# Kernel tuning notes

Measured on AMD Instinct MI355X. Metric: run time of the kernel, lower is better.

## Reference

```python
import jax, jax.numpy as jnp
import numpy as np

THRESHOLD = 1.0
CURRENT_DECAY = 0.5
VOLTAGE_DECAY = 0.5
WEIGHT_SCALE = 2.0  # slayer block weight_scale=2, weight_norm=False


def spike_fn(v):
    # Heaviside spike with hard threshold (forward only)
    return (v >= THRESHOLD).astype(v.dtype)


def conv_transpose_2d(x, w):
    # x: [NT, Cin, H, W]; w: [Cin, Cout, k, k] (pytorch ConvTranspose2d layout)
    # Equivalent dilated conv: swap in/out, flip spatial taps.
    rhs = jnp.transpose(w, (1, 0, 2, 3))[:, :, ::-1, ::-1]
    return jax.lax.conv_general_dilated(
        x, rhs, window_strides=(1, 1), padding=[(1, 1), (1, 1)],
        lhs_dilation=(2, 2), dimension_numbers=('NCHW', 'OIHW', 'NCHW'))


def cuba_block(x, w):
    # x: [N, Cin, H, W, T] -> spikes [N, Cout, 2H-1, 2W-1, T]
    N, Cin, H, W, T = x.shape
    xt = jnp.transpose(x, (4, 0, 1, 2, 3)).reshape(T * N, Cin, H, W)
    z = conv_transpose_2d(xt, WEIGHT_SCALE * w)  # synapse over all timesteps at once
    Cout, Ho, Wo = z.shape[1], z.shape[2], z.shape[3]
    z = z.reshape(T, N, Cout, Ho, Wo)

    def step(carry, zt):
        cur, vol = carry
        cur = (1.0 - CURRENT_DECAY) * cur + zt          # CUBA current dynamics
        vol = (1.0 - VOLTAGE_DECAY) * vol + cur          # CUBA voltage dynamics
        s = spike_fn(vol)
        vol = vol * (1.0 - s)                            # reset voltage on spike
        return (cur, vol), s

    init = (jnp.zeros_like(z[0]), jnp.zeros_like(z[0]))
    _, spikes = jax.lax.scan(step, init, z)              # [T, N, Cout, Ho, Wo]
    return jnp.transpose(spikes, (1, 2, 3, 4, 0))


def setup_inputs() -> dict:
    key = jax.random.key(0)
    k1, k2, k3, k4 = jax.random.split(key, 4)
    c_hid, C = 32, 2
    spike = (jax.random.uniform(k1, (4, c_hid * 4, 16, 16, 32)) < 0.3).astype(jnp.float32)

    def winit(k, cin, cout):
        return jax.random.normal(k, (cin, cout, 3, 3), jnp.float32) / np.sqrt(cin * 9.0)

    return {
        'spike': spike,
        'w1': winit(k2, c_hid * 4, c_hid * 2),
        'w2': winit(k3, c_hid * 2, c_hid),
        'w3': winit(k4, c_hid, C),
    }


def reference(spike, w1, w2, w3):
    counts = []
    for w in (w1, w2, w3):
        spike = cuba_block(spike, w)
        counts.append(jnp.mean(spike))
    return spike, jnp.stack(counts).reshape(1, -1)
```

## Files before the change

kernel.cpp:

```cpp
#include <hip/hip_runtime.h>

#define TT 32

__device__ __forceinline__ float bf16_bits_to_f32(unsigned short u) {
    unsigned v = ((unsigned)u) << 16; float f; __builtin_memcpy(&f, &v, 4); return f;
}
__device__ __forceinline__ unsigned short f32_to_bf16_rne(float f) {
    unsigned u; __builtin_memcpy(&u, &f, 4);
    u += 0x7FFFu + ((u >> 16) & 1u);
    return (unsigned short)(u >> 16);
}
__device__ __forceinline__ float round_bf16_f32(float f) {
    return bf16_bits_to_f32(f32_to_bf16_rne(f));
}
__device__ __forceinline__ float f64_to_bf16_f32(double d) {
    float fz = __double2float_rz(d);
    if ((double)fz != d) {
        unsigned u; __builtin_memcpy(&u, &fz, 4); u |= 1u; __builtin_memcpy(&fz, &u, 4);
    }
    return round_bf16_f32(fz);
}
__device__ __forceinline__ unsigned spread4(unsigned b) {
    unsigned x = (b | (b << 12)) & 0x000F000Fu;
    x = (x | (x << 6)) & 0x03030303u;
    x = (x | (x << 3)) & 0x11111111u;
    return x;
}

__global__ void detect_and_init(const unsigned* __restrict__ spk,
                                int* __restrict__ flag, float* __restrict__ sums)
{
    unsigned w = spk[threadIdx.x];
    bool ok = (w == 0u) || (w == 0x3F800000u);
    unsigned long long vote = __ballot(ok);
    if (threadIdx.x == 0) {
        flag[0] = (vote == 0xFFFFFFFFFFFFFFFFull) ? 0 : 1;
        sums[0] = 0.f; sums[1] = 0.f; sums[2] = 0.f;
    }
}

__global__ __launch_bounds__(256)
void pack_interleave(const void* __restrict__ ginv, unsigned* __restrict__ idx0,
                     const int* __restrict__ flag)
{
    const int gid = blockIdx.x * 256 + threadIdx.x;
    if (gid >= 32768) return;
    const int site = gid & 255;
    const int g    = (gid >> 8) & 31;
    const int n    = gid >> 13;

    unsigned m[4];
    #pragma unroll
    for (int k = 0; k < 4; ++k) {
        const size_t ebase = ((size_t)(n * 128 + 4 * g + k) * 256 + site) * TT;
        unsigned mask = 0u;
        if (flag[0]) {
            const uint4* p = (const uint4*)((const unsigned short*)ginv + ebase);
            #pragma unroll
            for (int q = 0; q < 4; ++q) {
                uint4 a = p[q];
                unsigned wd[4] = {a.x, a.y, a.z, a.w};
                #pragma unroll
                for (int mm = 0; mm < 4; ++mm) {
                    const int t = q * 8 + mm * 2;
                    mask |= (wd[mm] & 0xFFFFu) ? (1u << t)       : 0u;
                    mask |= (wd[mm] >> 16)     ? (1u << (t + 1)) : 0u;
                }
            }
        } else {
            const float4* p = (const float4*)((const float*)ginv + ebase);
            #pragma unroll
            for (int j = 0; j < 8; ++j) {
                float4 v = p[j];
                mask |= (v.x != 0.f) ? (1u << (j * 4 + 0)) : 0u;
                mask |= (v.y != 0.f) ? (1u << (j * 4 + 1)) : 0u;
                mask |= (v.z != 0.f) ? (1u << (j * 4 + 2)) : 0u;
                mask |= (v.w != 0.f) ? (1u << (j * 4 + 3)) : 0u;
            }
        }
        m[k] = mask;
    }
    #pragma unroll
    for (int q = 0; q < 4; ++q) {
        const unsigned w =  spread4((m[0] >> (8 * q)) & 0xFFu)
                         | (spread4((m[1] >> (8 * q)) & 0xFFu) << 1)
                         | (spread4((m[2] >> (8 * q)) & 0xFFu) << 2)
                         | (spread4((m[3] >> (8 * q)) & 0xFFu) << 3);
        idx0[q * 32768 + gid] = w;
    }
}

template<int C, int PLANE>
__global__ __launch_bounds__(256)
void pack_mid(const unsigned* __restrict__ masks, unsigned* __restrict__ idx)
{
    constexpr int G = C / 4;
    constexpr int TOT = 4 * G * PLANE;
    const int gid = blockIdx.x * 256 + threadIdx.x;
    if (gid >= TOT) return;
    const int site = gid % PLANE;
    const int g    = (gid / PLANE) % G;
    const int n    = gid / (PLANE * G);
    unsigned m[4];
    #pragma unroll
    for (int k = 0; k < 4; ++k)
        m[k] = masks[(n * C + 4 * g + k) * PLANE + site];
    #pragma unroll
    for (int q = 0; q < 4; ++q) {
        const unsigned w =  spread4((m[0] >> (8 * q)) & 0xFFu)
                         | (spread4((m[1] >> (8 * q)) & 0xFFu) << 1)
                         | (spread4((m[2] >> (8 * q)) & 0xFFu) << 2)
                         | (spread4((m[3] >> (8 * q)) & 0xFFu) << 3);
        idx[q * TOT + gid] = w;
    }
}

template<int CIN, int COUT, int MODE, bool LAST>
__global__ __launch_bounds__(256, 4)
void cuba_layer(const unsigned* __restrict__ idxIn, const void* __restrict__ wptr,
                void* __restrict__ goutv, unsigned* __restrict__ maskOut,
                int N, int Hi, int Wi, float* __restrict__ sumOut,
                const int* __restrict__ flag)
{
    constexpr int G = CIN / 4;
    constexpr int XW = (MODE == 1) ? 1536 : 1024;
    const bool isbf = (flag[0] != 0);
    const int Ho = 2 * Hi - 1, Wo = 2 * Wi - 1;
    const int co = (int)blockIdx.y;
    const int zz = 3 - (int)blockIdx.z;
    const int po = zz >> 1, pw = zz & 1;
    const int lg = po + pw;
    const int nTap = 1 << lg;
    const int nH = Hi - po, nW = Wi - pw;
    const int sites = N * nH * nW;
    const int lS = (MODE == 1) ? lg : ((zz == 3) ? 1 : 0);
    const int S  = 1 << lS;
    const int spb = 256 >> lS;
    const int siteBase = (int)blockIdx.x * spb;
    if (siteBase >= sites) return;

    __shared__ double lut[G][4][16];
    __shared__ double xch[XW];
    {
        const unsigned short* w16 = (const unsigned short*)wptr;
        const float* w32 = (const float*)wptr;
        const int entries = G * nTap * 16;
        for (int e = threadIdx.x; e < entries; e += 256) {
            const int idx = e & 15;
            const int tp  = (e >> 4) & (nTap - 1);
            const int g   = e >> (4 + lg);
            const int v = (po && (tp >= (pw ? 2 : 1))) ? 1 : 0;
            const int h = pw ? (tp & 1) : 0;
            const int kh = v ? 0 : (po ? 2 : 1);
            const int kw = h ? 0 : (pw ? 2 : 1);
            const int wof = kh * 3 + kw;
            double s = 0.0;
            #pragma unroll
            for (int k = 0; k < 4; ++k) {
                if ((idx >> k) & 1) {
                    const int wi = ((4 * g + k) * COUT + co) * 9 + wof;
                    const float wraw = isbf ? bf16_bits_to_f32(w16[wi]) : w32[wi];
                    s += 2.0 * (double)wraw;
                }
            }
            lut[g][tp][idx] = s;
        }
    }
    __syncthreads();

    const int slab = (int)threadIdx.x >> (8 - lS);
    const int sl   = (int)threadIdx.x & (spb - 1);
    const int siteIdx = siteBase + sl;
    const bool valid = siteIdx < sites;
    const int sIdx = valid ? siteIdx : 0;

    const int b  = sIdx % nW;
    const int t1v = sIdx / nW;
    const int a  = t1v % nH;
    const int n  = t1v / nH;
    const int oh = 2 * a + po, ow = 2 * b + pw;
    const int plane = Hi * Wi;
    const int QT = N * G * plane;

    const int siteA = a * Wi + b;
    const int siteB = siteA + 1;
    const int siteC = siteA + Wi;
    const int siteD = siteC + 1;

    int s1 = siteA, tp1 = 0, s2 = 0, tp2 = 0;
    bool two = false;
    if (MODE == 0) {
        if (zz == 3) {
            if (slab == 0) { s1 = siteA; tp1 = 0; s2 = siteB; tp2 = 1; two = true; }
            else           { s1 = siteC; tp1 = 2; s2 = siteD; tp2 = 3; two = true; }
        } else if (zz == 1) { s2 = siteB; tp2 = 1; two = true; }
        else if (zz == 2)   { s2 = siteC; tp2 = 1; two = true; }
    } else {
        if (zz == 1)      { if (slab == 1) { s1 = siteB; tp1 = 1; } }
        else if (zz == 2) { if (slab == 1) { s1 = siteC; tp1 = 1; } }
        else if (zz == 3) {
            if      (slab == 1) { s1 = siteB; tp1 = 1; }
            else if (slab == 2) { s1 = siteC; tp1 = 2; }
            else if (slab == 3) { s1 = siteD; tp1 = 3; }
        }
    }

    unsigned mask = 0u;
    float  curF = 0.f, volF = 0.f;
    double curD = 0.0, volD = 0.0;
    float cnt = 0.f;

    #pragma unroll 1
    for (int p = 0; p < 4; ++p) {
        double acc[8];
        #pragma unroll
        for (int j = 0; j < 8; ++j) acc[j] = 0.0;

        const unsigned* pb = idxIn + (size_t)p * QT + (size_t)(n * G) * plane;
        #pragma unroll 4
        for (int g = 0; g < G; ++g) {
            const unsigned* bp = pb + (size_t)g * plane;
            const unsigned w1 = bp[s1];
            #pragma unroll
            for (int j = 0; j < 8; ++j)
                acc[j] += lut[g][tp1][(w1 >> (4 * j)) & 0xFu];
            if (two) {
                const unsigned w2 = bp[s2];
                #pragma unroll
                for (int j = 0; j < 8; ++j)
                    acc[j] += lut[g][tp2][(w2 >> (4 * j)) & 0xFu];
            }
        }

        if (S > 1) {
            if (slab != 0) {
                #pragma unroll
                for (int j = 0; j < 8; ++j)
                    xch[(slab - 1) * (8 * spb) + j * spb + sl] = acc[j];
            }
            __syncthreads();
            if (slab == 0) {
                for (int s = 1; s < S; ++s)
                    #pragma unroll
                    for (int j = 0; j < 8; ++j)
                        acc[j] += xch[(s - 1) * (8 * spb) + j * spb + sl];
            }
        }

        if (slab == 0) {
            if (isbf) {
                #pragma unroll
                for (int j = 0; j < 8; ++j) {
                    const int t = p * 8 + j;
                    const float z = f64_to_bf16_f32(acc[j]);
                    curF = round_bf16_f32(0.5f * curF + z);
                    volF = round_bf16_f32(0.5f * volF + curF);
                    const bool fire = (volF >= 1.0f);
                    mask |= fire ? (1u << t) : 0u;
                    volF = fire ? 0.f : volF;
                }
            } else {
                #pragma unroll
                for (int j = 0; j < 8; ++j) {
                    const int t = p * 8 + j;
                    curD = fma(0.5, curD, acc[j]);
                    volD = fma(0.5, volD, curD);
                    const bool fire = (volD >= 1.0);
                    mask |= fire ? (1u << t) : 0u;
                    volD = fire ? 0.0 : volD;
                }
            }
        }
        if (S > 1) __syncthreads();
    }

    if (slab == 0 && valid) {
        cnt = (float)__popc(mask);
        const int gidOut = ((n * COUT + co) * Ho + oh) * Wo + ow;
        if (LAST) {
            if (isbf) {
                uint4* ob = (uint4*)((unsigned short*)goutv + (size_t)gidOut * TT);
                #pragma unroll
                for (int q = 0; q < 4; ++q) {
                    unsigned wd[4];
                    #pragma unroll
                    for (int m2 = 0; m2 < 4; ++m2) {
                        const int t = (q * 4 + m2) * 2;
                        wd[m2] = (((mask >> t) & 1u) ? 0x3F80u : 0u)
                               | (((mask >> (t + 1)) & 1u) ? 0x3F800000u : 0u);
                    }
                    ob[q] = make_uint4(wd[0], wd[1], wd[2], wd[3]);
                }
            } else {
                float4* ob = (float4*)((float*)goutv + (size_t)gidOut * TT);
                #pragma unroll
                for (int j = 0; j < 8; ++j) {
                    float4 s4;
                    s4.x = (mask >> (j * 4 + 0)) & 1u ? 1.0f : 0.0f;
                    s4.y = (mask >> (j * 4 + 1)) & 1u ? 1.0f : 0.0f;
                    s4.z = (mask >> (j * 4 + 2)) & 1u ? 1.0f : 0.0f;
                    s4.w = (mask >> (j * 4 + 3)) & 1u ? 1.0f : 0.0f;
                    ob[j] = s4;
                }
            }
        } else {
            maskOut[gidOut] = mask;
        }
    }

    #pragma unroll
    for (int o = 32; o >= 1; o >>= 1) cnt += __shfl_down(cnt, o);
    if ((threadIdx.x & 63) == 0 && cnt > 0.f) atomicAdd(sumOut, cnt);
}

__global__ void finalize_counts(const float* __restrict__ sums,
                                void* __restrict__ out, const int* __restrict__ flag)
{
    int i = threadIdx.x;
    if (i < 3) {
        const float numel[3] = {7872512.f, 15239168.f, 3748096.f};
        float v = sums[i] / numel[i];
        if (flag[0]) ((unsigned short*)out)[3748096 + i] = f32_to_bf16_rne(v);
        else         ((float*)out)[3748096 + i] = v;
    }
}

extern "C" void kernel_launch(void* const* d_in, const int* in_sizes, int n_in,
                              void* d_out, int out_size, void* d_ws, size_t ws_size,
                              hipStream_t stream)
{
    const void* x  = d_in[0];
    const void* w1 = d_in[1];
    const void* w2 = d_in[2];
    const void* w3 = d_in[3];

    unsigned* bufA = (unsigned*)d_ws;
    unsigned* bufB = bufA + 476288;
    unsigned* idx0 = bufB;
    float* sums = (float*)(bufB + 476288);
    int*   flag = (int*)(sums + 3);

    detect_and_init<<<1, 64, 0, stream>>>((const unsigned*)x, flag, sums);
    pack_interleave<<<128, 256, 0, stream>>>(x, idx0, flag);

    cuba_layer<128, 64, 0, false><<<dim3(8, 64, 4), 256, 0, stream>>>(
        idx0, w1, nullptr, bufA, 4, 16, 16, sums + 0, flag);
    pack_mid<64, 961><<<241, 256, 0, stream>>>(bufA, bufB);
    cuba_layer<64, 32, 0, false><<<dim3(29, 32, 4), 256, 0, stream>>>(
        bufB, w2, nullptr, bufA, 4, 31, 31, sums + 1, flag);
    pack_mid<32, 3721><<<466, 256, 0, stream>>>(bufA, bufB);
    cuba_layer<32, 2, 1, true><<<dim3(225, 2, 4), 256, 0, stream>>>(
        bufB, w3, d_out, nullptr, 4, 61, 61, sums + 2, flag);

    finalize_counts<<<1, 64, 0, stream>>>(sums, d_out, flag);
}
```

Before: 423.6 us.

## Process all taps per thread with paired 16-timestep packed words for first two layers

Layers 1 and 2 now use a new kernel in which each thread handles one output site and accumulates every tap itself. This removes the slab split and the shared-memory exchange of partial sums. Input spike words are stored as uint2 pairs so each load covers 16 timesteps and the loop runs two passes instead of four. The change cuts block syncs and shared traffic, but each thread now carries 16 double accumulators, which raises register pressure and lowers parallelism per block. The last layer keeps the slab kernel with single-word packing.

```diff
diff --git a/kernel.cpp b/kernel.cpp
--- a/kernel.cpp
+++ b/kernel.cpp
@@ -80,19 +80,20 @@
         }
         m[k] = mask;
     }
-    #pragma unroll
-    for (int q = 0; q < 4; ++q) {
-        const unsigned w =  spread4((m[0] >> (8 * q)) & 0xFFu)
-                         | (spread4((m[1] >> (8 * q)) & 0xFFu) << 1)
-                         | (spread4((m[2] >> (8 * q)) & 0xFFu) << 2)
-                         | (spread4((m[3] >> (8 * q)) & 0xFFu) << 3);
-        idx0[q * 32768 + gid] = w;
-    }
+    unsigned w[4];
+    #pragma unroll
+    for (int q = 0; q < 4; ++q)
+        w[q] =  spread4((m[0] >> (8 * q)) & 0xFFu)
+             | (spread4((m[1] >> (8 * q)) & 0xFFu) << 1)
+             | (spread4((m[2] >> (8 * q)) & 0xFFu) << 2)
+             | (spread4((m[3] >> (8 * q)) & 0xFFu) << 3);
+    *(uint2*)(idx0 + (size_t)gid * 2)           = make_uint2(w[0], w[1]);
+    *(uint2*)(idx0 + (size_t)(32768 + gid) * 2) = make_uint2(w[2], w[3]);
 }
 
 template<int C, int PLANE>
 __global__ __launch_bounds__(256)
-void pack_mid(const unsigned* __restrict__ masks, unsigned* __restrict__ idx)
+void pack_mid_pairs(const unsigned* __restrict__ masks, unsigned* __restrict__ idx)
 {
     constexpr int G = C / 4;
     constexpr int TOT = 4 * G * PLANE;
@@ -105,6 +106,32 @@
     #pragma unroll
     for (int k = 0; k < 4; ++k)
         m[k] = masks[(n * C + 4 * g + k) * PLANE + site];
+    unsigned w[4];
+    #pragma unroll
+    for (int q = 0; q < 4; ++q)
+        w[q] =  spread4((m[0] >> (8 * q)) & 0xFFu)
+             | (spread4((m[1] >> (8 * q)) & 0xFFu) << 1)
+             | (spread4((m[2] >> (8 * q)) & 0xFFu) << 2)
+             | (spread4((m[3] >> (8 * q)) & 0xFFu) << 3);
+    *(uint2*)(idx + (size_t)gid * 2)         = make_uint2(w[0], w[1]);
+    *(uint2*)(idx + (size_t)(TOT + gid) * 2) = make_uint2(w[2], w[3]);
+}
+
+template<int C, int PLANE>
+__global__ __launch_bounds__(256)
+void pack_mid(const unsigned* __restrict__ masks, unsigned* __restrict__ idx)
+{
+    constexpr int G = C / 4;
+    constexpr int TOT = 4 * G * PLANE;
+    const int gid = blockIdx.x * 256 + threadIdx.x;
+    if (gid >= TOT) return;
+    const int site = gid % PLANE;
+    const int g    = (gid / PLANE) % G;
+    const int n    = gid / (PLANE * G);
+    unsigned m[4];
+    #pragma unroll
+    for (int k = 0; k < 4; ++k)
+        m[k] = masks[(n * C + 4 * g + k) * PLANE + site];
     #pragma unroll
     for (int q = 0; q < 4; ++q) {
         const unsigned w =  spread4((m[0] >> (8 * q)) & 0xFFu)
@@ -115,15 +142,13 @@
     }
 }
 
-template<int CIN, int COUT, int MODE, bool LAST>
-__global__ __launch_bounds__(256, 4)
-void cuba_layer(const unsigned* __restrict__ idxIn, const void* __restrict__ wptr,
-                void* __restrict__ goutv, unsigned* __restrict__ maskOut,
-                int N, int Hi, int Wi, float* __restrict__ sumOut,
-                const int* __restrict__ flag)
+template<int CIN, int COUT>
+__global__ __launch_bounds__(256)
+void cuba_layer2(const unsigned* __restrict__ idxIn, const void* __restrict__ wptr,
+                 unsigned* __restrict__ maskOut, int N, int Hi, int Wi,
+                 float* __restrict__ sumOut, const int* __restrict__ flag)
 {
     constexpr int G = CIN / 4;
-    constexpr int XW = (MODE == 1) ? 1536 : 1024;
     const bool isbf = (flag[0] != 0);
     const int Ho = 2 * Hi - 1, Wo = 2 * Wi - 1;
     const int co = (int)blockIdx.y;
@@ -133,14 +158,10 @@
     const int nTap = 1 << lg;
     const int nH = Hi - po, nW = Wi - pw;
     const int sites = N * nH * nW;
-    const int lS = (MODE == 1) ? lg : ((zz == 3) ? 1 : 0);
-    const int S  = 1 << lS;
-    const int spb = 256 >> lS;
-    const int siteBase = (int)blockIdx.x * spb;
+    const int siteBase = (int)blockIdx.x * 256;
     if (siteBase >= sites) return;
 
     __shared__ double lut[G][4][16];
-    __shared__ double xch[XW];
     {
         const unsigned short* w16 = (const unsigned short*)wptr;
         const float* w32 = (const float*)wptr;
@@ -168,6 +189,139 @@
     }
     __syncthreads();
 
+    const int siteIdx = siteBase + (int)threadIdx.x;
+    float cnt = 0.f;
+
+    if (siteIdx < sites) {
+        const int b  = siteIdx % nW;
+        const int t1 = siteIdx / nW;
+        const int a  = t1 % nH;
+        const int n  = t1 / nH;
+        const int oh = 2 * a + po, ow = 2 * b + pw;
+        const int plane = Hi * Wi;
+        const int QT = N * G * plane;
+
+        const int siteA = a * Wi + b;
+        const int siteB = siteA + 1;
+        const int siteC = siteA + Wi;
+        const int siteD = siteC + 1;
+
+        unsigned mask = 0u;
+        float  curF = 0.f, volF = 0.f;
+        double curD = 0.0, volD = 0.0;
+
+        #pragma unroll 1
+        for (int p = 0; p < 2; ++p) {
+            double acc[16];
+            #pragma unroll
+            for (int j = 0; j < 16; ++j) acc[j] = 0.0;
+
+            const unsigned* pb = idxIn + (size_t)(p * QT + n * G * plane) * 2;
+            for (int g = 0; g < G; ++g) {
+                const unsigned* bp = pb + (size_t)g * plane * 2;
+
+                auto doTap = [&](int site, int tp) {
+                    const uint2 wv = *(const uint2*)(bp + (size_t)site * 2);
+                    const double* lp = &lut[g][tp][0];
+                    #pragma unroll
+                    for (int j = 0; j < 8; ++j)
+                        acc[j] += lp[(wv.x >> (4 * j)) & 0xFu];
+                    #pragma unroll
+                    for (int j = 0; j < 8; ++j)
+                        acc[8 + j] += lp[(wv.y >> (4 * j)) & 0xFu];
+                };
+
+                doTap(siteA, 0);
+                if (pw) doTap(siteB, 1);
+                if (po) {
+                    doTap(siteC, pw ? 2 : 1);
+                    if (pw) doTap(siteD, 3);
+                }
+            }
+
+            if (isbf) {
+                #pragma unroll
+                for (int j = 0; j < 16; ++j) {
+                    const int t = p * 16 + j;
+                    const float z = f64_to_bf16_f32(acc[j]);
+                    curF = round_bf16_f32(0.5f * curF + z);
+                    volF = round_bf16_f32(0.5f * volF + curF);
+                    const bool fire = (volF >= 1.0f);
+                    mask |= fire ? (1u << t) : 0u;
+                    volF = fire ? 0.f : volF;
+                }
+            } else {
+                #pragma unroll
+                for (int j = 0; j < 16; ++j) {
+                    const int t = p * 16 + j;
+                    curD = fma(0.5, curD, acc[j]);
+                    volD = fma(0.5, volD, curD);
+                    const bool fire = (volD >= 1.0);
+                    mask |= fire ? (1u << t) : 0u;
+                    volD = fire ? 0.0 : volD;
+                }
+            }
+        }
+        cnt = (float)__popc(mask);
+        maskOut[((n * COUT + co) * Ho + oh) * Wo + ow] = mask;
+    }
+
+    #pragma unroll
+    for (int o = 32; o >= 1; o >>= 1) cnt += __shfl_down(cnt, o);
+    if ((threadIdx.x & 63) == 0 && cnt > 0.f) atomicAdd(sumOut, cnt);
+}
+
+template<int CIN, int COUT>
+__global__ __launch_bounds__(256)
+void cuba_layer_slab(const unsigned* __restrict__ idxIn, const void* __restrict__ wptr,
+                     void* __restrict__ goutv, int N, int Hi, int Wi,
+                     float* __restrict__ sumOut, const int* __restrict__ flag)
+{
+    constexpr int G = CIN / 4;
+    const bool isbf = (flag[0] != 0);
+    const int Ho = 2 * Hi - 1, Wo = 2 * Wi - 1;
+    const int co = (int)blockIdx.y;
+    const int zz = 3 - (int)blockIdx.z;
+    const int po = zz >> 1, pw = zz & 1;
+    const int lg = po + pw;
+    const int nTap = 1 << lg;
+    const int nH = Hi - po, nW = Wi - pw;
+    const int sites = N * nH * nW;
+    const int lS = lg;
+    const int S  = 1 << lS;
+    const int spb = 256 >> lS;
+    const int siteBase = (int)blockIdx.x * spb;
+    if (siteBase >= sites) return;
+
+    __shared__ double lut[G][4][16];
+    __shared__ double xch[1536];
+    {
+        const unsigned short* w16 = (const unsigned short*)wptr;
+        const float* w32 = (const float*)wptr;
+        const int entries = G * nTap * 16;
+        for (int e = threadIdx.x; e < entries; e += 256) {
+            const int idx = e & 15;
+            const int tp  = (e >> 4) & (nTap - 1);
+            const int g   = e >> (4 + lg);
+            const int v = (po && (tp >= (pw ? 2 : 1))) ? 1 : 0;
+            const int h = pw ? (tp & 1) : 0;
+            const int kh = v ? 0 : (po ? 2 : 1);
+            const int kw = h ? 0 : (pw ? 2 : 1);
+            const int wof = kh * 3 + kw;
+            double s = 0.0;
+            #pragma unroll
+            for (int k = 0; k < 4; ++k) {
+                if ((idx >> k) & 1) {
+                    const int wi = ((4 * g + k) * COUT + co) * 9 + wof;
+                    const float wraw = isbf ? bf16_bits_to_f32(w16[wi]) : w32[wi];
+                    s += 2.0 * (double)wraw;
+                }
+            }
+            lut[g][tp][idx] = s;
+        }
+    }
+    __syncthreads();
+
     const int slab = (int)threadIdx.x >> (8 - lS);
     const int sl   = (int)threadIdx.x & (spb - 1);
     const int siteIdx = siteBase + sl;
@@ -187,22 +341,13 @@
     const int siteC = siteA + Wi;
     const int siteD = siteC + 1;
 
-    int s1 = siteA, tp1 = 0, s2 = 0, tp2 = 0;
-    bool two = false;
-    if (MODE == 0) {
-        if (zz == 3) {
-            if (slab == 0) { s1 = siteA; tp1 = 0; s2 = siteB; tp2 = 1; two = true; }
-            else           { s1 = siteC; tp1 = 2; s2 = siteD; tp2 = 3; two = true; }
-        } else if (zz == 1) { s2 = siteB; tp2 = 1; two = true; }
-        else if (zz == 2)   { s2 = siteC; tp2 = 1; two = true; }
-    } else {
-        if (zz == 1)      { if (slab == 1) { s1 = siteB; tp1 = 1; } }
-        else if (zz == 2) { if (slab == 1) { s1 = siteC; tp1 = 1; } }
-        else if (zz == 3) {
-            if      (slab == 1) { s1 = siteB; tp1 = 1; }
-            else if (slab == 2) { s1 = siteC; tp1 = 2; }
-            else if (slab == 3) { s1 = siteD; tp1 = 3; }
-        }
+    int s1 = siteA, tp1 = 0;
+    if (zz == 1)      { if (slab == 1) { s1 = siteB; tp1 = 1; } }
+    else if (zz == 2) { if (slab == 1) { s1 = siteC; tp1 = 1; } }
+    else if (zz == 3) {
+        if      (slab == 1) { s1 = siteB; tp1 = 1; }
+        else if (slab == 2) { s1 = siteC; tp1 = 2; }
+        else if (slab == 3) { s1 = siteD; tp1 = 3; }
     }
 
     unsigned mask = 0u;
@@ -217,19 +362,11 @@
         for (int j = 0; j < 8; ++j) acc[j] = 0.0;
 
         const unsigned* pb = idxIn + (size_t)p * QT + (size_t)(n * G) * plane;
-        #pragma unroll 4
         for (int g = 0; g < G; ++g) {
-            const unsigned* bp = pb + (size_t)g * plane;
-            const unsigned w1 = bp[s1];
+            const unsigned w1 = pb[(size_t)g * plane + s1];
             #pragma unroll
             for (int j = 0; j < 8; ++j)
                 acc[j] += lut[g][tp1][(w1 >> (4 * j)) & 0xFu];
-            if (two) {
-                const unsigned w2 = bp[s2];
-                #pragma unroll
-                for (int j = 0; j < 8; ++j)
-                    acc[j] += lut[g][tp2][(w2 >> (4 * j)) & 0xFu];
-            }
         }
 
         if (S > 1) {
@@ -277,34 +414,30 @@
     if (slab == 0 && valid) {
         cnt = (float)__popc(mask);
         const int gidOut = ((n * COUT + co) * Ho + oh) * Wo + ow;
-        if (LAST) {
-            if (isbf) {
-                uint4* ob = (uint4*)((unsigned short*)goutv + (size_t)gidOut * TT);
-                #pragma unroll
-                for (int q = 0; q < 4; ++q) {
-                    unsigned wd[4];
-                    #pragma unroll
-                    for (int m2 = 0; m2 < 4; ++m2) {
-                        const int t = (q * 4 + m2) * 2;
-                        wd[m2] = (((mask >> t) & 1u) ? 0x3F80u : 0u)
-                               | (((mask >> (t + 1)) & 1u) ? 0x3F800000u : 0u);
-                    }
-                    ob[q] = make_uint4(wd[0], wd[1], wd[2], wd[3]);
-                }
-            } else {
-                float4* ob = (float4*)((float*)goutv + (size_t)gidOut * TT);
-                #pragma unroll
-                for (int j = 0; j < 8; ++j) {
-                    float4 s4;
-                    s4.x = (mask >> (j * 4 + 0)) & 1u ? 1.0f : 0.0f;
-                    s4.y = (mask >> (j * 4 + 1)) & 1u ? 1.0f : 0.0f;
-                    s4.z = (mask >> (j * 4 + 2)) & 1u ? 1.0f : 0.0f;
-                    s4.w = (mask >> (j * 4 + 3)) & 1u ? 1.0f : 0.0f;
-                    ob[j] = s4;
-                }
+        if (isbf) {
+            uint4* ob = (uint4*)((unsigned short*)goutv + (size_t)gidOut * TT);
+            #pragma unroll
+            for (int q = 0; q < 4; ++q) {
+                unsigned wd[4];
+                #pragma unroll
+                for (int m2 = 0; m2 < 4; ++m2) {
+                    const int t = (q * 4 + m2) * 2;
+                    wd[m2] = (((mask >> t) & 1u) ? 0x3F80u : 0u)
+                           | (((mask >> (t + 1)) & 1u) ? 0x3F800000u : 0u);
+                }
+                ob[q] = make_uint4(wd[0], wd[1], wd[2], wd[3]);
             }
         } else {
-            maskOut[gidOut] = mask;
+            float4* ob = (float4*)((float*)goutv + (size_t)gidOut * TT);
+            #pragma unroll
+            for (int j = 0; j < 8; ++j) {
+                float4 s4;
+                s4.x = (mask >> (j * 4 + 0)) & 1u ? 1.0f : 0.0f;
+                s4.y = (mask >> (j * 4 + 1)) & 1u ? 1.0f : 0.0f;
+                s4.z = (mask >> (j * 4 + 2)) & 1u ? 1.0f : 0.0f;
+                s4.w = (mask >> (j * 4 + 3)) & 1u ? 1.0f : 0.0f;
+                ob[j] = s4;
+            }
         }
     }
 
@@ -343,14 +476,14 @@
     detect_and_init<<<1, 64, 0, stream>>>((const unsigned*)x, flag, sums);
     pack_interleave<<<128, 256, 0, stream>>>(x, idx0, flag);
 
-    cuba_layer<128, 64, 0, false><<<dim3(8, 64, 4), 256, 0, stream>>>(
-        idx0, w1, nullptr, bufA, 4, 16, 16, sums + 0, flag);
-    pack_mid<64, 961><<<241, 256, 0, stream>>>(bufA, bufB);
-    cuba_layer<64, 32, 0, false><<<dim3(29, 32, 4), 256, 0, stream>>>(
-        bufB, w2, nullptr, bufA, 4, 31, 31, sums + 1, flag);
+    cuba_layer2<128, 64><<<dim3(4, 64, 4), 256, 0, stream>>>(
+        idx0, w1, bufA, 4, 16, 16, sums + 0, flag);
+    pack_mid_pairs<64, 961><<<241, 256, 0, stream>>>(bufA, bufB);
+    cuba_layer2<64, 32><<<dim3(16, 32, 4), 256, 0, stream>>>(
+        bufB, w2, bufA, 4, 31, 31, sums + 1, flag);
     pack_mid<32, 3721><<<466, 256, 0, stream>>>(bufA, bufB);
-    cuba_layer<32, 2, 1, true><<<dim3(225, 2, 4), 256, 0, stream>>>(
-        bufB, w3, d_out, nullptr, 4, 61, 61, sums + 2, flag);
+    cuba_layer_slab<32, 2><<<dim3(225, 2, 4), 256, 0, stream>>>(
+        bufB, w3, d_out, 4, 61, 61, sums + 2, flag);
 
     finalize_counts<<<1, 64, 0, stream>>>(sums, d_out, flag);
 }
```

New measurement: 419.7 us. About the same (-0.9%).
